# Kernel optimization log

Hardware: AMD Instinct MI355X
Metric: run time of the kernel (lower is better)

Reference implementation:

```python
import jax, jax.numpy as jnp
import numpy as np

B, S, D_IN, D_OUT = 2, 4096, 512, 512


def setup_inputs() -> dict:
    key = jax.random.key(0)
    k1, k2, k3, k4 = jax.random.split(key, 4)
    x = jax.random.normal(k1, (B, S, D_IN), dtype=jnp.float32)
    # weights stored as [d_in, d_out] so projection is x @ W
    W_query = jax.random.normal(k2, (D_IN, D_OUT), dtype=jnp.float32) * (D_IN ** -0.5)
    W_key = jax.random.normal(k3, (D_IN, D_OUT), dtype=jnp.float32) * (D_IN ** -0.5)
    W_value = jax.random.normal(k4, (D_IN, D_OUT), dtype=jnp.float32) * (D_IN ** -0.5)
    return {"x": x, "W_query": W_query, "W_key": W_key, "W_value": W_value}


def reference(x, W_query, W_key, W_value):
    # Faithful to source: masked_fill is called non-in-place and its result
    # discarded, so NO causal mask is actually applied. Dropout prob = 0.0.
    d_out = W_query.shape[-1]
    q = jnp.einsum('bsi,io->bso', x, W_query)  # [B,S,D_OUT]
    k = jnp.einsum('bsi,io->bso', x, W_key)
    v = jnp.einsum('bsi,io->bso', x, W_value)
    scores = jnp.einsum('bqd,bkd->bqk', q, k) / jnp.sqrt(jnp.float32(d_out))
    weights = jax.nn.softmax(scores, axis=-1)  # [B,S,S]
    context = jnp.einsum('bqk,bkd->bqd', weights, v)  # [B,S,D_OUT]
    return context
```

## Files before the change

kernel.cpp:

```cpp
#include <hip/hip_runtime.h>
#include <cstdint>
#include <cstddef>

typedef unsigned short u16;
typedef __attribute__((ext_vector_type(8))) short bf16x8;
typedef __attribute__((ext_vector_type(4))) float f32x4;

struct alignas(8) u16x4_t { u16 x, y, z, w; };

__device__ __forceinline__ u16 f2bf(float f) {
  uint32_t u = __builtin_bit_cast(uint32_t, f);
  u += 0x7FFFu + ((u >> 16) & 1u);
  return (u16)(u >> 16);
}
__device__ __forceinline__ float bf2f(u16 h) {
  uint32_t u = ((uint32_t)h) << 16;
  return __builtin_bit_cast(float, u);
}

__device__ __forceinline__ void g2l16(const u16* g, u16* l) {
  __builtin_amdgcn_global_load_lds(
      (const __attribute__((address_space(1))) void*)g,
      (__attribute__((address_space(3))) void*)l, 16, 0, 0);
}

#define S_WAITCNT_VM(N) \
  __builtin_amdgcn_s_waitcnt((((N) & 0xF)) | (0x7 << 4) | (0xF << 8) | ((((N) >> 4) & 3) << 14))

template <int DEPTH, int BM, int BN>
__device__ __forceinline__ void gemm_bt_pipe(
    const u16* __restrict__ A, const u16* __restrict__ Bt,
    int lda, int ldb, int kIters, int m0, int n0,
    u16* sh, f32x4 (&acc)[BM / 32][BN / 32]) {
  constexpr int MI = BM / 32;
  constexpr int NI = BN / 32;
  constexpr int T = (BM + BN) / 64;
  constexpr int SLOT = (BM + BN) * 32;
  const int tid = threadIdx.x;
  const int lane = tid & 63, wave = tid >> 6;
  const int wm = wave >> 1, wn = wave & 1, lr = lane & 15, quad = lane >> 4;

  const u16* gp[T];
#pragma unroll
  for (int t = 0; t < T; ++t) {
    const int c = t * 256 + wave * 64 + lane;
    if (c < BM * 4) {
      const int r = c >> 2;
      const int s = (c & 3) ^ ((r >> 1) & 3);
      gp[t] = A + (size_t)(m0 + r) * lda + s * 8;
    } else {
      const int cb = c - BM * 4;
      const int r = cb >> 2;
      const int s = (cb & 3) ^ ((r >> 1) & 3);
      gp[t] = Bt + (size_t)(n0 + r) * ldb + s * 8;
    }
  }
  const int wo = wave * 512;

  auto issue = [&](int slot, int kb) {
    u16* s = sh + slot * SLOT;
#pragma unroll
    for (int t = 0; t < T; ++t)
      g2l16(gp[t] + kb, s + t * 2048 + wo);
  };

#pragma unroll
  for (int p = 0; p < DEPTH; ++p)
    issue(p, (p < kIters ? p : kIters - 1) * 32);

  const int xq = (quad ^ ((lr >> 1) & 3)) * 8;
  const int arow = wm * (BM / 2) + lr;
  const int brow = wn * (BN / 2) + lr;

  bf16x8 af[MI], b0[NI], b1[NI];
  S_WAITCNT_VM(T * (DEPTH - 1));
  __builtin_amdgcn_s_barrier();
#pragma unroll
  for (int ni = 0; ni < NI; ++ni)
    b0[ni] = *(const bf16x8*)(sh + BM * 32 + ((brow + ni * 16) * 32 + xq));
#pragma unroll
  for (int mi = 0; mi < MI; ++mi)
    af[mi] = *(const bf16x8*)(sh + ((arow + mi * 16) * 32 + xq));

  auto step = [&](int kt, bf16x8 (&bc)[NI], bf16x8 (&bn)[NI]) {
    S_WAITCNT_VM(T * (DEPTH - 2));
    __builtin_amdgcn_s_barrier();
    const int nx = (kt + 1 < kIters) ? kt + 1 : kIters - 1;
    u16* s1 = sh + (nx % DEPTH) * SLOT;
#pragma unroll
    for (int ni = 0; ni < NI; ++ni)
      bn[ni] = *(const bf16x8*)(s1 + BM * 32 + ((brow + ni * 16) * 32 + xq));
    __builtin_amdgcn_s_setprio(1);
#pragma unroll
    for (int mi = 0; mi < MI; ++mi) {
#pragma unroll
      for (int ni = 0; ni < NI; ++ni)
        acc[mi][ni] = __builtin_amdgcn_mfma_f32_16x16x32_bf16(af[mi], bc[ni], acc[mi][ni], 0, 0, 0);
      af[mi] = *(const bf16x8*)(s1 + ((arow + mi * 16) * 32 + xq));
    }
    __builtin_amdgcn_s_setprio(0);
    __builtin_amdgcn_s_barrier();
    const int kn = kt + DEPTH;
    issue(kn % DEPTH, (kn < kIters ? kn : kIters - 1) * 32);
  };

  for (int kt = 0; kt + 2 <= kIters; kt += 2) {
    step(kt, b0, b1);
    step(kt + 1, b1, b0);
  }
}

template <int DEPTH, int BM, int BN>
__device__ __forceinline__ void gemm_bt_pipe_w8(
    const u16* __restrict__ A, const u16* __restrict__ Bt,
    int lda, int ldb, int kIters, int m0, int n0,
    u16* sh, f32x4 (&acc)[BM / 32][BN / 64]) {
  constexpr int MI = BM / 32;
  constexpr int NI = BN / 64;
  constexpr int T = (BM + BN) / 128;
  constexpr int SLOT = (BM + BN) * 32;
  const int tid = threadIdx.x;
  const int lane = tid & 63, wave = tid >> 6;
  const int wm = wave >> 2, wn = wave & 3, lr = lane & 15, quad = lane >> 4;

  const u16* gp[T];
#pragma unroll
  for (int t = 0; t < T; ++t) {
    const int c = t * 512 + wave * 64 + lane;
    if (c < BM * 4) {
      const int r = c >> 2;
      const int s = (c & 3) ^ ((r >> 1) & 3);
      gp[t] = A + (size_t)(m0 + r) * lda + s * 8;
    } else {
      const int cb = c - BM * 4;
      const int r = cb >> 2;
      const int s = (cb & 3) ^ ((r >> 1) & 3);
      gp[t] = Bt + (size_t)(n0 + r) * ldb + s * 8;
    }
  }
  const int wo = wave * 512;

  auto issue = [&](int slot, int kb) {
    u16* s = sh + slot * SLOT;
#pragma unroll
    for (int t = 0; t < T; ++t)
      g2l16(gp[t] + kb, s + t * 4096 + wo);
  };

#pragma unroll
  for (int p = 0; p < DEPTH; ++p)
    issue(p, (p < kIters ? p : kIters - 1) * 32);

  const int xq = (quad ^ ((lr >> 1) & 3)) * 8;
  const int arow = wm * (BM / 2) + lr;
  const int brow = wn * (BN / 4) + lr;

  bf16x8 af[MI], b0[NI], b1[NI];
  S_WAITCNT_VM(T * (DEPTH - 1));
  __builtin_amdgcn_s_barrier();
#pragma unroll
  for (int ni = 0; ni < NI; ++ni)
    b0[ni] = *(const bf16x8*)(sh + BM * 32 + ((brow + ni * 16) * 32 + xq));
#pragma unroll
  for (int mi = 0; mi < MI; ++mi)
    af[mi] = *(const bf16x8*)(sh + ((arow + mi * 16) * 32 + xq));

  auto step = [&](int kt, bf16x8 (&bc)[NI], bf16x8 (&bn)[NI]) {
    S_WAITCNT_VM(T * (DEPTH - 2));
    __builtin_amdgcn_s_barrier();
    const int nx = (kt + 1 < kIters) ? kt + 1 : kIters - 1;
    u16* s1 = sh + (nx % DEPTH) * SLOT;
#pragma unroll
    for (int ni = 0; ni < NI; ++ni)
      bn[ni] = *(const bf16x8*)(s1 + BM * 32 + ((brow + ni * 16) * 32 + xq));
    __builtin_amdgcn_s_setprio(1);
#pragma unroll
    for (int mi = 0; mi < MI; ++mi) {
#pragma unroll
      for (int ni = 0; ni < NI; ++ni)
        acc[mi][ni] = __builtin_amdgcn_mfma_f32_16x16x32_bf16(af[mi], bc[ni], acc[mi][ni], 0, 0, 0);
      af[mi] = *(const bf16x8*)(s1 + ((arow + mi * 16) * 32 + xq));
    }
    __builtin_amdgcn_s_setprio(0);
    __builtin_amdgcn_s_barrier();
    const int kn = kt + DEPTH;
    issue(kn % DEPTH, (kn < kIters ? kn : kIters - 1) * 32);
  };

  for (int kt = 0; kt + 2 <= kIters; kt += 2) {
    step(kt, b0, b1);
    step(kt + 1, b1, b0);
  }
}

#define ZERO_ACC4(acc)                        \
  _Pragma("unroll") for (int mi = 0; mi < 4; ++mi) \
  _Pragma("unroll") for (int ni = 0; ni < 4; ++ni) \
      acc[mi][ni] = f32x4{0.f, 0.f, 0.f, 0.f};

template <int MI>
__device__ __forceinline__ void epilogue_ct16(
    const f32x4 (&acc)[MI][4], u16* __restrict__ base, int m0w, int n0w,
    int ld, int lane, bool do_exp, float scale, float* rs) {
  const int lr = lane & 15, quad = lane >> 4;
  const int j = quad >> 1, par = quad & 1;
#pragma unroll
  for (int mp = 0; mp < MI / 2; ++mp) {
#pragma unroll
    for (int ni = 0; ni < 4; ++ni) {
      uint32_t p0[2], p1[2];
#pragma unroll
      for (int h = 0; h < 2; ++h) {
        const f32x4 v = acc[mp * 2 + h][ni];
        float e0, e1, e2, e3;
        if (do_exp) {
          e0 = __expf(v[0] * scale); e1 = __expf(v[1] * scale);
          e2 = __expf(v[2] * scale); e3 = __expf(v[3] * scale);
        } else {
          e0 = v[0]; e1 = v[1]; e2 = v[2]; e3 = v[3];
        }
        const u16 h0 = f2bf(e0), h1 = f2bf(e1), h2 = f2bf(e2), h3 = f2bf(e3);
        p0[h] = (uint32_t)h0 | ((uint32_t)h1 << 16);
        p1[h] = (uint32_t)h2 | ((uint32_t)h3 << 16);
        if (rs) rs[ni] += bf2f(h0) + bf2f(h1) + bf2f(h2) + bf2f(h3);
      }
      const uint32_t s0 = par ? p0[0] : p0[1];
      const uint32_t s1 = par ? p1[0] : p1[1];
      const uint32_t r0 = (uint32_t)__shfl_xor((int)s0, 16);
      const uint32_t r1 = (uint32_t)__shfl_xor((int)s1, 16);
      uint4 st;
      if (!par) { st.x = p0[0]; st.y = p1[0]; st.z = r0;    st.w = r1;    }
      else      { st.x = r0;    st.y = r1;    st.z = p0[1]; st.w = p1[1]; }
      const int m = m0w + 16 * (mp * 2 + par) + 8 * j;
      const int n = n0w + ni * 16 + lr;
      *(uint4*)(base + (size_t)n * ld + m) = st;
    }
  }
}

__global__ __launch_bounds__(256) void prep_kernel(
    const float* __restrict__ x, u16* __restrict__ Xb,
    const float* __restrict__ W0, const float* __restrict__ W1,
    const float* __restrict__ W2, u16* __restrict__ Wt,
    float* __restrict__ L) {
  __shared__ float tile[32][33];
  const int id = blockIdx.x;
  if (id < 4096) {
    const int i = (id * 256 + threadIdx.x) * 4;
    const float4 v = *(const float4*)(x + i);
    u16x4_t h;
    h.x = f2bf(v.x); h.y = f2bf(v.y); h.z = f2bf(v.z); h.w = f2bf(v.w);
    *(u16x4_t*)(Xb + i) = h;
    return;
  }
  if (id >= 4864) {
    L[(id - 4864) * 256 + threadIdx.x] = 0.f;
    return;
  }
  const int t = id - 4096;
  const int wz = t >> 8, rem = t & 255;
  const float* W = wz == 0 ? W0 : (wz == 1 ? W1 : W2);
  u16* out = Wt + (size_t)wz * 512 * 512;
  const int bx = (rem & 15) * 32;
  const int by = (rem >> 4) * 32;
  const int tx = threadIdx.x & 31, ty = threadIdx.x >> 5;
#pragma unroll
  for (int i = 0; i < 32; i += 8)
    tile[ty + i][tx] = W[(size_t)(by + ty + i) * 512 + bx + tx];
  __syncthreads();
#pragma unroll
  for (int i = 0; i < 32; i += 8)
    out[(size_t)(bx + ty + i) * 512 + by + tx] = f2bf(tile[tx][ty + i]);
}

__global__ __launch_bounds__(256) void qkv_kernel(
    const u16* __restrict__ Xb, const u16* __restrict__ Wt,
    u16* __restrict__ Qb, u16* __restrict__ Kb, u16* __restrict__ Vt) {
  __shared__ u16 sh[3 * 8192];
  const int z = blockIdx.z;
  int m0, n0;
  const u16 *A, *Bt;
  if (z < 2) {
    m0 = blockIdx.y * 128;
    n0 = blockIdx.x * 128;
    A = Wt + (size_t)z * 512 * 512;
    Bt = Xb;
  } else {
    m0 = blockIdx.x * 128;
    n0 = blockIdx.y * 128;
    A = Xb;
    Bt = Wt + (size_t)2 * 512 * 512;
  }
  f32x4 acc[4][4];
  ZERO_ACC4(acc);
  gemm_bt_pipe<3, 128, 128>(A, Bt, 512, 512, 16, m0, n0, sh, acc);

  const int lane = threadIdx.x & 63, wave = threadIdx.x >> 6;
  const int wm = wave >> 1, wn = wave & 1;
  if (z < 2) {
    epilogue_ct16<4>(acc, z == 0 ? Qb : Kb, m0 + wm * 64, n0 + wn * 64, 512,
                     lane, false, 1.f, nullptr);
  } else {
    const int bb = m0 >> 12;
    epilogue_ct16<4>(acc, Vt + (size_t)bb * 512 * 4096,
                     (m0 & 4095) + wm * 64, n0 + wn * 64, 4096,
                     lane, false, 1.f, nullptr);
  }
}

__global__ __launch_bounds__(512, 2) void scores_kernel(
    const u16* __restrict__ Qb, const u16* __restrict__ Kb,
    u16* __restrict__ P, float* __restrict__ L) {
  extern __shared__ u16 sh[];
  const int id = blockIdx.x;
  const int b = id >> 8;
  const int r = id & 255;
  const int j = r >> 3;
  const int qx = (r & 7) * 2 + (j >> 4);
  const int ky = j & 15;
  const int m0 = ky * 256;
  const int n0 = qx * 256;
  f32x4 acc[8][4];
#pragma unroll
  for (int mi = 0; mi < 8; ++mi)
#pragma unroll
    for (int ni = 0; ni < 4; ++ni)
      acc[mi][ni] = f32x4{0.f, 0.f, 0.f, 0.f};
  gemm_bt_pipe_w8<4, 256, 256>(Kb + (size_t)b * 4096 * 512,
                               Qb + (size_t)b * 4096 * 512,
                               512, 512, 16, m0, n0, sh, acc);

  const int lane = threadIdx.x & 63, wave = threadIdx.x >> 6;
  const int wm = wave >> 2, wn = wave & 3, lr = lane & 15, quad = lane >> 4;
  const float scale = 0.04419417382415922f;
  u16* Pb = P + (size_t)b * 4096 * 4096;

  float rs[4] = {0.f, 0.f, 0.f, 0.f};
  epilogue_ct16<8>(acc, Pb, m0 + wm * 128, n0 + wn * 64, 4096, lane, true,
                   scale, rs);

#pragma unroll
  for (int ni = 0; ni < 4; ++ni) {
    float v = rs[ni];
    v += __shfl_xor(v, 16);
    v += __shfl_xor(v, 32);
    if (quad == 0)
      atomicAdd(&L[b * 4096 + n0 + wn * 64 + ni * 16 + lr], v);
  }
}

__global__ __launch_bounds__(256) void pv_kernel(
    const u16* __restrict__ P, const u16* __restrict__ Vt,
    float* __restrict__ part0, float* __restrict__ out) {
  __shared__ u16 sh[3 * 8192];
  const int b = blockIdx.z;
  const int id = blockIdx.x;
  const int ntile = (id >> 3) & 3;
  const int rest = (id & 7) | ((id >> 5) << 3);
  const int mtile = rest & 31;
  const int ks = rest >> 5;
  const int m0 = mtile * 128;
  const int n0 = ntile * 128;
  const int k0 = ks * 2048;
  f32x4 acc[4][4];
  ZERO_ACC4(acc);
  gemm_bt_pipe<3, 128, 128>(P + (size_t)b * 4096 * 4096 + k0,
                            Vt + (size_t)b * 512 * 4096 + k0,
                            4096, 4096, 64, m0, n0, sh, acc);

  const int lane = threadIdx.x & 63, wave = threadIdx.x >> 6;
  const int wm = wave >> 1, wn = wave & 1, lr = lane & 15, quad = lane >> 4;
  float* dst = ks ? out : part0;
#pragma unroll
  for (int mi = 0; mi < 4; ++mi) {
    const int row = m0 + wm * 64 + mi * 16 + quad * 4;
#pragma unroll
    for (int ni = 0; ni < 4; ++ni) {
      const int col = n0 + wn * 64 + ni * 16 + lr;
#pragma unroll
      for (int i = 0; i < 4; ++i)
        dst[(size_t)b * 2097152 + (size_t)(row + i) * 512 + col] = acc[mi][ni][i];
    }
  }
}

__global__ __launch_bounds__(256) void reduce_kernel(
    const float* __restrict__ part0, const float* __restrict__ L,
    float* __restrict__ out) {
  const int i = (blockIdx.x * 256 + threadIdx.x) * 4;
  const float rinv = 1.0f / L[i >> 9];
  const float4 a = *(const float4*)(out + i);
  const float4 p = *(const float4*)(part0 + i);
  float4 r;
  r.x = (a.x + p.x) * rinv; r.y = (a.y + p.y) * rinv;
  r.z = (a.z + p.z) * rinv; r.w = (a.w + p.w) * rinv;
  *(float4*)(out + i) = r;
}

extern "C" void kernel_launch(void* const* d_in, const int* in_sizes, int n_in,
                              void* d_out, int out_size, void* d_ws, size_t ws_size,
                              hipStream_t stream) {
  const float* x  = (const float*)d_in[0];
  const float* Wq = (const float*)d_in[1];
  const float* Wk = (const float*)d_in[2];
  const float* Wv = (const float*)d_in[3];
  float* out = (float*)d_out;
  char* ws = (char*)d_ws;
  u16* Xb = (u16*)(ws);
  u16* Qb = (u16*)(ws + 8388608);
  u16* Kb = (u16*)(ws + 16777216);
  u16* Vt = (u16*)(ws + 25165824);
  u16* Wt = (u16*)(ws + 33554432);
  u16* P  = (u16*)(ws + 35127296);
  float* L = (float*)(ws + 102236160);
  float* part0 = (float*)(ws + 8388608);

  static bool attr_set = false;
  if (!attr_set) {
    hipFuncSetAttribute(reinterpret_cast<const void*>(scores_kernel),
                        hipFuncAttributeMaxDynamicSharedMemorySize, 131072);
    attr_set = true;
  }

  prep_kernel<<<4896, 256, 0, stream>>>(x, Xb, Wq, Wk, Wv, Wt, L);
  qkv_kernel<<<dim3(64, 4, 3), 256, 0, stream>>>(Xb, Wt, Qb, Kb, Vt);
  scores_kernel<<<512, 512, 131072, stream>>>(Qb, Kb, P, L);
  pv_kernel<<<dim3(256, 1, 2), 256, 0, stream>>>(P, Vt, part0, out);
  reduce_kernel<<<4096, 256, 0, stream>>>(part0, L, out);
}
```

Baseline: 190.5 us.

## Restructure scores GEMM into 3-slot, 4-phase pipeline with split prefetch

Replaces the 4-deep LDS pipeline of the scores-kernel GEMM with a 3-slot ring buffer. Each k-step is split into two phases: load A/B fragments, issue half of the next global->LDS copies, run half of the MFMAs, then repeat for the second half. This interleaves prefetch issue with compute and drops dynamic shared memory from 128KB to 96KB, which may help occupancy or scheduling. In exchange it adds more barriers per k-iteration and removes the register double-buffering of fragments, so LDS-read latency is exposed before each MFMA batch.

```diff
diff --git a/kernel.cpp b/kernel.cpp
--- a/kernel.cpp
+++ b/kernel.cpp
@@ -26,6 +26,7 @@
 
 #define S_WAITCNT_VM(N) \
   __builtin_amdgcn_s_waitcnt((((N) & 0xF)) | (0x7 << 4) | (0xF << 8) | ((((N) >> 4) & 3) << 14))
+#define S_WAITCNT_LGKM0 __builtin_amdgcn_s_waitcnt(0xC07F)
 
 template <int DEPTH, int BM, int BN>
 __device__ __forceinline__ void gemm_bt_pipe(
@@ -110,13 +111,11 @@
   }
 }
 
-template <int DEPTH, int BM, int BN>
-__device__ __forceinline__ void gemm_bt_pipe_w8(
+template <int BM, int BN>
+__device__ __forceinline__ void gemm_bt_8w_4ph(
     const u16* __restrict__ A, const u16* __restrict__ Bt,
     int lda, int ldb, int kIters, int m0, int n0,
     u16* sh, f32x4 (&acc)[BM / 32][BN / 64]) {
-  constexpr int MI = BM / 32;
-  constexpr int NI = BN / 64;
   constexpr int T = (BM + BN) / 128;
   constexpr int SLOT = (BM + BN) * 32;
   const int tid = threadIdx.x;
@@ -140,56 +139,62 @@
   }
   const int wo = wave * 512;
 
-  auto issue = [&](int slot, int kb) {
-    u16* s = sh + slot * SLOT;
+#pragma unroll
+  for (int p = 0; p < 2; ++p)
 #pragma unroll
     for (int t = 0; t < T; ++t)
-      g2l16(gp[t] + kb, s + t * 4096 + wo);
-  };
-
-#pragma unroll
-  for (int p = 0; p < DEPTH; ++p)
-    issue(p, (p < kIters ? p : kIters - 1) * 32);
+      g2l16(gp[t] + p * 32, sh + p * SLOT + t * 4096 + wo);
+  S_WAITCNT_VM(4);
+  __builtin_amdgcn_s_barrier();
 
   const int xq = (quad ^ ((lr >> 1) & 3)) * 8;
-  const int arow = wm * (BM / 2) + lr;
-  const int brow = wn * (BN / 4) + lr;
-
-  bf16x8 af[MI], b0[NI], b1[NI];
-  S_WAITCNT_VM(T * (DEPTH - 1));
-  __builtin_amdgcn_s_barrier();
-#pragma unroll
-  for (int ni = 0; ni < NI; ++ni)
-    b0[ni] = *(const bf16x8*)(sh + BM * 32 + ((brow + ni * 16) * 32 + xq));
-#pragma unroll
-  for (int mi = 0; mi < MI; ++mi)
-    af[mi] = *(const bf16x8*)(sh + ((arow + mi * 16) * 32 + xq));
-
-  auto step = [&](int kt, bf16x8 (&bc)[NI], bf16x8 (&bn)[NI]) {
-    S_WAITCNT_VM(T * (DEPTH - 2));
-    __builtin_amdgcn_s_barrier();
-    const int nx = (kt + 1 < kIters) ? kt + 1 : kIters - 1;
-    u16* s1 = sh + (nx % DEPTH) * SLOT;
-#pragma unroll
-    for (int ni = 0; ni < NI; ++ni)
-      bn[ni] = *(const bf16x8*)(s1 + BM * 32 + ((brow + ni * 16) * 32 + xq));
+  const int abase = (wm * (BM / 2) + lr) * 32 + xq;
+  const int bbase = BM * 32 + (wn * (BN / 4) + lr) * 32 + xq;
+
+  int si = 0, s2 = 2;
+  for (int kt = 0; kt < kIters; ++kt) {
+    u16* slot = sh + si * SLOT;
+    const int kn = kt + 2;
+    const int kb = (kn < kIters ? kn : kIters - 1) * 32;
+    u16* st = sh + s2 * SLOT + wo;
+
+    bf16x8 a0[4], b0[4];
+#pragma unroll
+    for (int i = 0; i < 4; ++i)
+      a0[i] = *(const bf16x8*)(slot + abase + i * 512);
+#pragma unroll
+    for (int j = 0; j < 4; ++j)
+      b0[j] = *(const bf16x8*)(slot + bbase + j * 512);
+    g2l16(gp[0] + kb, st);
+    g2l16(gp[1] + kb, st + 4096);
+    __builtin_amdgcn_s_barrier();
+    S_WAITCNT_LGKM0;
     __builtin_amdgcn_s_setprio(1);
 #pragma unroll
-    for (int mi = 0; mi < MI; ++mi) {
-#pragma unroll
-      for (int ni = 0; ni < NI; ++ni)
-        acc[mi][ni] = __builtin_amdgcn_mfma_f32_16x16x32_bf16(af[mi], bc[ni], acc[mi][ni], 0, 0, 0);
-      af[mi] = *(const bf16x8*)(s1 + ((arow + mi * 16) * 32 + xq));
-    }
+    for (int i = 0; i < 4; ++i)
+#pragma unroll
+      for (int j = 0; j < 4; ++j)
+        acc[i][j] = __builtin_amdgcn_mfma_f32_16x16x32_bf16(a0[i], b0[j], acc[i][j], 0, 0, 0);
     __builtin_amdgcn_s_setprio(0);
     __builtin_amdgcn_s_barrier();
-    const int kn = kt + DEPTH;
-    issue(kn % DEPTH, (kn < kIters ? kn : kIters - 1) * 32);
-  };
-
-  for (int kt = 0; kt + 2 <= kIters; kt += 2) {
-    step(kt, b0, b1);
-    step(kt + 1, b1, b0);
+#pragma unroll
+    for (int i = 0; i < 4; ++i)
+      a0[i] = *(const bf16x8*)(slot + abase + (4 + i) * 512);
+    g2l16(gp[2] + kb, st + 8192);
+    g2l16(gp[3] + kb, st + 12288);
+    __builtin_amdgcn_s_barrier();
+    S_WAITCNT_LGKM0;
+    __builtin_amdgcn_s_setprio(1);
+#pragma unroll
+    for (int i = 0; i < 4; ++i)
+#pragma unroll
+      for (int j = 0; j < 4; ++j)
+        acc[4 + i][j] = __builtin_amdgcn_mfma_f32_16x16x32_bf16(a0[i], b0[j], acc[4 + i][j], 0, 0, 0);
+    __builtin_amdgcn_s_setprio(0);
+    S_WAITCNT_VM(4);
+    __builtin_amdgcn_s_barrier();
+    si = si == 2 ? 0 : si + 1;
+    s2 = s2 == 2 ? 0 : s2 + 1;
   }
 }
 
@@ -326,9 +331,9 @@
 #pragma unroll
     for (int ni = 0; ni < 4; ++ni)
       acc[mi][ni] = f32x4{0.f, 0.f, 0.f, 0.f};
-  gemm_bt_pipe_w8<4, 256, 256>(Kb + (size_t)b * 4096 * 512,
-                               Qb + (size_t)b * 4096 * 512,
-                               512, 512, 16, m0, n0, sh, acc);
+  gemm_bt_8w_4ph<256, 256>(Kb + (size_t)b * 4096 * 512,
+                           Qb + (size_t)b * 4096 * 512,
+                           512, 512, 16, m0, n0, sh, acc);
 
   const int lane = threadIdx.x & 63, wave = threadIdx.x >> 6;
   const int wm = wave >> 2, wn = wave & 3, lr = lane & 15, quad = lane >> 4;
@@ -418,13 +423,13 @@
   static bool attr_set = false;
   if (!attr_set) {
     hipFuncSetAttribute(reinterpret_cast<const void*>(scores_kernel),
-                        hipFuncAttributeMaxDynamicSharedMemorySize, 131072);
+                        hipFuncAttributeMaxDynamicSharedMemorySize, 98304);
     attr_set = true;
   }
 
   prep_kernel<<<4896, 256, 0, stream>>>(x, Xb, Wq, Wk, Wv, Wt, L);
   qkv_kernel<<<dim3(64, 4, 3), 256, 0, stream>>>(Xb, Wt, Qb, Kb, Vt);
-  scores_kernel<<<512, 512, 131072, stream>>>(Qb, Kb, P, L);
+  scores_kernel<<<512, 512, 98304, stream>>>(Qb, Kb, P, L);
   pv_kernel<<<dim3(256, 1, 2), 256, 0, stream>>>(P, Vt, part0, out);
   reduce_kernel<<<4096, 256, 0, stream>>>(part0, L, out);
 }
```

Result: no change. 189.9 us (-0.3%).
